# Optimization experiments

Hardware: AMD Instinct MI355X
Metric: run time of the kernel (lower is better)

Reference implementation:

```python
import jax, jax.numpy as jnp
import numpy as np

N = 100000; E = 200000; H = 64; P2 = 250000; P3 = 500000; G = 2048; NC = 10
NF = 18; EF = 18; Y = 0.25; EPS_BN = 1e-5


def setup_inputs() -> dict:
    key = jax.random.key(0)
    ks = jax.random.split(key, 20)
    def rn(i, shape, s=0.05):
        return jax.random.normal(ks[i], shape, jnp.float32) * s
    inp = {}
    inp["x"] = jax.random.normal(ks[0], (N, NF), jnp.float32)
    inp["edge_attr"] = jax.random.normal(ks[1], (E, EF), jnp.float32)
    inp["paths2"] = jax.random.randint(ks[2], (P2, 2), 0, N, jnp.int32)
    inp["ei2"] = jax.random.randint(ks[3], (P2, 1), 0, E, jnp.int32)
    inp["paths3"] = jax.random.randint(ks[4], (P3, 3), 0, N, jnp.int32)
    inp["ei3"] = jax.random.randint(ks[5], (P3, 2), 0, E, jnp.int32)
    inp["batch"] = jnp.sort(jax.random.randint(ks[6], (N,), 0, G, jnp.int32))
    inp["w_feat"] = rn(7, (NF, H)); inp["b_feat"] = jnp.zeros((H,), jnp.float32)
    inp["w_bond"] = rn(8, (EF, H)); inp["b_bond"] = jnp.zeros((H,), jnp.float32)
    inp["w_ih"] = rn(9, (4 * H, 2 * H)); inp["w_hh"] = rn(10, (4 * H, H))
    inp["b_ih"] = jnp.zeros((4 * H,), jnp.float32); inp["b_hh"] = jnp.zeros((4 * H,), jnp.float32)
    inp["bn_g"] = jnp.ones((2, H), jnp.float32); inp["bn_b"] = jnp.zeros((2, H), jnp.float32)
    inp["mlp_w1"] = rn(11, (2, H, H)); inp["mlp_b1"] = jnp.zeros((2, H), jnp.float32)
    inp["bn1_g"] = jnp.ones((2, H), jnp.float32); inp["bn1_b"] = jnp.zeros((2, H), jnp.float32)
    inp["mlp_w2"] = rn(12, (2, H, H)); inp["mlp_b2"] = jnp.zeros((2, H), jnp.float32)
    inp["bn2_g"] = jnp.ones((2, H), jnp.float32); inp["bn2_b"] = jnp.zeros((2, H), jnp.float32)
    inp["w_att"] = rn(13, (H,)); inp["b_att"] = jnp.zeros((1,), jnp.float32)
    inp["w_l1"] = rn(14, (H, H)); inp["b_l1"] = jnp.zeros((H,), jnp.float32)
    inp["w_l2"] = rn(15, (H, NC)); inp["b_l2"] = jnp.zeros((NC,), jnp.float32)
    return inp


def _batch_norm(x, g, b):
    # training-mode BN: biased batch statistics, eps=1e-5 (torch BatchNorm1d)
    m = x.mean(axis=0)
    v = x.var(axis=0)
    return (x - m) * jax.lax.rsqrt(v + EPS_BN) * g + b


def _lstm_final(x_seq, w_ih, w_hh, b_ih, b_hh):
    # x_seq: [P, L, 2H]; torch LSTM gate order i,f,g,o; return final hidden [P, H]
    P = x_seq.shape[0]
    Hd = w_hh.shape[1]
    def step(carry, xt):
        h, c = carry
        gates = xt @ w_ih.T + b_ih + h @ w_hh.T + b_hh
        i, f, g, o = jnp.split(gates, 4, axis=-1)
        c = jax.nn.sigmoid(f) * c + jax.nn.sigmoid(i) * jnp.tanh(g)
        h = jax.nn.sigmoid(o) * jnp.tanh(c)
        return (h, c), None
    h0 = jnp.zeros((P, Hd), x_seq.dtype)
    (h, _), _ = jax.lax.scan(step, (h0, h0), jnp.swapaxes(x_seq, 0, 1))
    return h


def _conv(i, x_in, ea_enc, paths, ei, w_ih, w_hh, b_ih, b_hh, bn_g, bn_b,
          mlp_w1, mlp_b1, bn1_g, bn1_b, mlp_w2, mlp_b2, bn2_g, bn2_b):
    P = paths.shape[0]
    ea = ea_enc[ei]                                        # [P, L-1, H]
    ea = jnp.concatenate([jnp.zeros((P, 1, H), ea.dtype), ea], axis=1)  # [P, L, H]
    x_cat = jnp.concatenate([x_in[paths], ea], axis=-1)    # [P, L, 2H]
    h = _lstm_final(x_cat, w_ih, w_hh, b_ih, b_hh)         # [P, H]
    h = jax.ops.segment_sum(h, paths[:, -1], num_segments=N)  # scatter_add to nodes
    h = _batch_norm(h, bn_g[i], bn_b[i])                   # residuals=False
    h = jax.nn.relu(_batch_norm(h @ mlp_w1[i] + mlp_b1[i], bn1_g[i], bn1_b[i]))
    h = jax.nn.relu(_batch_norm(h @ mlp_w2[i] + mlp_b2[i], bn2_g[i], bn2_b[i]))
    return h


def _attention(query, keys, w_att, b_att):
    scores = []
    for k in keys:
        s = jnp.sum(query * k, axis=0)                     # [H], sum over nodes
        s = (s - s.min()) / (s.max() - s.min() + 1e-6)
        scores.append(s @ w_att + b_att[0])                # scalar
    w = jax.nn.softmax(jnp.stack(scores))                  # [K]
    rep = sum(k * w[j] for j, k in enumerate(keys))
    return rep + query


def _forward(x, edge_attr, w_feat, b_feat, w_bond, b_bond, w_ih, w_hh, b_ih, b_hh,
             bn_g, bn_b, mlp_w1, mlp_b1, bn1_g, bn1_b, mlp_w2, mlp_b2, bn2_g, bn2_b,
             w_att, b_att, w_l1, b_l1, w_l2, b_l2, paths2, ei2, paths3, ei3, batch):
    W0 = x @ w_feat + b_feat                               # [N, H]
    ea_enc = edge_attr @ w_bond + b_bond                   # [E, H]
    common = (w_ih, w_hh, b_ih, b_hh, bn_g, bn_b, mlp_w1, mlp_b1, bn1_g, bn1_b,
              mlp_w2, mlp_b2, bn2_g, bn2_b)
    W1 = _conv(0, W0, ea_enc, paths2, ei2, *common)
    Win = (1.0 - Y) * W0 - Y * W1
    W2 = _conv(1, Win, ea_enc, paths3, ei3, *common)
    out = _attention(W0, [W1, W2], w_att, b_att)           # [N, H]
    out = jax.ops.segment_sum(out, batch, num_segments=G)  # global_add_pool -> [G, H]
    out = jax.nn.relu(out @ w_l1 + b_l1)
    return out @ w_l2 + b_l2                               # [G, NC]


def reference(x, edge_attr, paths2, ei2, paths3, ei3, batch, w_feat, b_feat,
              w_bond, b_bond, w_ih, w_hh, b_ih, b_hh, bn_g, bn_b, mlp_w1, mlp_b1,
              bn1_g, bn1_b, mlp_w2, mlp_b2, bn2_g, bn2_b, w_att, b_att,
              w_l1, b_l1, w_l2, b_l2):
    return _forward(x, edge_attr, w_feat, b_feat, w_bond, b_bond, w_ih, w_hh, b_ih, b_hh,
                    bn_g, bn_b, mlp_w1, mlp_b1, bn1_g, bn1_b, mlp_w2, mlp_b2, bn2_g, bn2_b,
                    w_att, b_att, w_l1, b_l1, w_l2, b_l2, paths2, ei2, paths3, ei3, batch)
```

## Files before the change

kernel.cpp:

```cpp
#include <hip/hip_runtime.h>
#include <math.h>

#define NNODES 100000
#define NEDGES 200000
#define HD 64
#define NP2 250000
#define NP3 500000
#define NG 2048
#define NCLS 10
#define NFEAT 18
#define EFEAT 18

typedef short short8v __attribute__((ext_vector_type(8)));
typedef float f32x4 __attribute__((ext_vector_type(4)));

__device__ __forceinline__ unsigned short bf16r(float a) {
    unsigned u = __builtin_bit_cast(unsigned, a);
    return (unsigned short)((u + 0x7FFFu + ((u >> 16) & 1u)) >> 16);
}

#define LOG2E 1.4426950408889634f

__global__ void prep_all(const float* __restrict__ w_ih, const float* __restrict__ w_hh,
                         const float* __restrict__ b_ih, const float* __restrict__ b_hh,
                         unsigned short* __restrict__ Bp, float* __restrict__ bsum,
                         float* __restrict__ zsmall, float* __restrict__ pooled) {
    int b = blockIdx.x;
    int t = threadIdx.x;
    if (b < 192) {
        int gid = b * 256 + t;
        int kc = gid >> 13;
        int rem = gid & 8191;
        int nt = rem >> 9;
        int rem2 = rem & 511;
        int l = rem2 >> 3, j = rem2 & 7;
        int c = l & 15, q = l >> 4;
        int jh = nt >> 2, qg = nt & 3;
        int k = kc * 32 + q * 8 + j;
        int n = qg * 64 + 16 * jh + c;
        float f = (k < 128) ? w_ih[n * 128 + k] : w_hh[n * 64 + (k - 128)];
        float s = (qg == 2) ? 2.f * LOG2E : LOG2E;
        Bp[gid] = bf16r(f * s);
    } else if (b == 192) {
        float s = ((t >> 6) == 2) ? 2.f * LOG2E : LOG2E;
        bsum[t] = (b_ih[t] + b_hh[t]) * s;
        for (int i = t; i < 960; i += 256) zsmall[i] = 0.f;
    } else {
        pooled[(b - 193) * 256 + t] = 0.f;
    }
}

__global__ void encode_all(const float* __restrict__ X, const float* __restrict__ Wf,
                           const float* __restrict__ bf,
                           const float* __restrict__ Ea, const float* __restrict__ Wb,
                           const float* __restrict__ bb,
                           float* __restrict__ W0, unsigned short* __restrict__ W0b,
                           unsigned short* __restrict__ eab) {
    long gid = (long)blockIdx.x * 256 + threadIdx.x;
    if (gid >= (long)(NNODES + NEDGES) * 64) return;
    long r = gid >> 6;
    int col = (int)(gid & 63);
    if (r < NNODES) {
        float acc = bf[col];
        const float* xr = X + r * NFEAT;
        for (int k = 0; k < NFEAT; ++k) acc += xr[k] * Wf[k * 64 + col];
        W0[gid] = acc;
        W0b[gid] = bf16r(acc);
    } else {
        long r2 = r - NNODES;
        float acc = bb[col];
        const float* xr = Ea + r2 * EFEAT;
        for (int k = 0; k < EFEAT; ++k) acc += xr[k] * Wb[k * 64 + col];
        eab[r2 * 64 + col] = bf16r(acc);
    }
}

template <int L>
__global__ __launch_bounds__(256, 3)
void conv_mfma(const unsigned short* __restrict__ xb, const unsigned short* __restrict__ eab,
               const int* __restrict__ paths, const int* __restrict__ ei,
               const unsigned short* __restrict__ Bp, const float* __restrict__ bsum,
               float* __restrict__ hsum, int P) {
    __shared__ unsigned short Al[2][64 * 200];

    const int t = threadIdx.x;
    const int w = t >> 6, lane = t & 63;
    const int c = lane & 15, q = lane >> 4;
    const int pl = t >> 2, gq = t & 3;
    const long pg = (long)blockIdx.x * 64 + pl;
    const int pc = (pg < P) ? (int)pg : P - 1;

    const short8v* __restrict__ Bv = (const short8v*)Bp;
    const int bbase = w * 256 + lane;

    short8v Bk0[4];
#pragma unroll
    for (int g2 = 0; g2 < 4; ++g2) Bk0[g2] = Bv[g2 * 64 + bbase];
    f32x4 bfr[4];
#pragma unroll
    for (int g2 = 0; g2 < 4; ++g2) {
        float b = bsum[g2 * 64 + 16 * w + c];
        f32x4 v; v[0] = b; v[1] = b; v[2] = b; v[3] = b;
        bfr[g2] = v;
    }

    float creg[16];
#pragma unroll
    for (int i = 0; i < 16; ++i) creg[i] = 0.f;

    f32x4 acc[4][4];
    short8v s0[4], s1[4];
    uint4 nu0, nu1, ev0, ev1;

    {
        int node = paths[pc * L + 0];
        const uint4* s4 = (const uint4*)(xb + (size_t)node * HD);
        *(uint4*)&Al[0][pl * 200 + gq * 16] = s4[2 * gq];
        *(uint4*)&Al[0][pl * 200 + gq * 16 + 8] = s4[2 * gq + 1];
    }
    __syncthreads();

#define LOADB(BUF, KC)                                                         \
        { _Pragma("unroll")                                                    \
          for (int g2 = 0; g2 < 4; ++g2)                                       \
              BUF[g2] = Bv[(KC) * 1024 + g2 * 64 + bbase]; }

#define CHUNKB(BUF, KC)                                                        \
        { _Pragma("unroll")                                                    \
          for (int mt = 0; mt < 4; ++mt) {                                     \
              short8v af = *(const short8v*)&Ac[(mt * 16 + c) * 200 + (KC) * 32 + q * 8]; \
              _Pragma("unroll")                                                \
              for (int g2 = 0; g2 < 4; ++g2)                                   \
                  acc[mt][g2] = __builtin_amdgcn_mfma_f32_16x16x32_bf16(       \
                      af, BUF[g2], bfr[g2], 0, 0, 0);                          \
          } }

#define CHUNKS(BUF, KC)                                                        \
        { _Pragma("unroll")                                                    \
          for (int mt = 0; mt < 4; ++mt) {                                     \
              short8v af = *(const short8v*)&Ac[(mt * 16 + c) * 200 + (KC) * 32 + q * 8]; \
              _Pragma("unroll")                                                \
              for (int g2 = 0; g2 < 4; ++g2)                                   \
                  acc[mt][g2] = __builtin_amdgcn_mfma_f32_16x16x32_bf16(       \
                      af, BUF[g2], acc[mt][g2], 0, 0, 0);                      \
          } }

    int cur = 0;
    for (int step = 0; step < L; ++step) {
        const unsigned short* Ac = Al[cur];
        unsigned short* An = Al[cur ^ 1];

        if (step == 0) {
            LOADB(s0, 1)
            CHUNKB(Bk0, 0)
            CHUNKS(s0, 1)
        } else {
            LOADB(s0, 1) LOADB(s1, 2)
            CHUNKB(Bk0, 0)
            CHUNKS(s0, 1) LOADB(s0, 3)
            CHUNKS(s1, 2) LOADB(s1, 4)
            CHUNKS(s0, 3) LOADB(s0, 5)
            CHUNKS(s1, 4)
            CHUNKS(s0, 5)
        }

        if (step + 1 < L) {
            int node = paths[pc * L + step + 1];
            const uint4* s4 = (const uint4*)(xb + (size_t)node * HD);
            nu0 = s4[2 * gq]; nu1 = s4[2 * gq + 1];
            int e = ei[pc * (L - 1) + step];
            const uint4* e4 = (const uint4*)(eab + (size_t)e * HD);
            ev0 = e4[2 * gq]; ev1 = e4[2 * gq + 1];
        }

#pragma unroll
        for (int mt = 0; mt < 4; ++mt) {
#pragma unroll
            for (int r = 0; r < 4; ++r) {
                float gi = acc[mt][0][r], gf = acc[mt][1][r];
                float gg = acc[mt][2][r], go = acc[mt][3][r];
                float ea = __builtin_amdgcn_exp2f(-gf);
                float eb = __builtin_amdgcn_exp2f(-gi);
                float ed = __builtin_amdgcn_exp2f(-gg);
                float eo = __builtin_amdgcn_exp2f(-go);
                float pa = 1.f + ea, pb = 1.f + eb, pd = 1.f + ed;
                float cn = (creg[mt * 4 + r] * pb * pd + (1.f - ed) * pa) *
                           __builtin_amdgcn_rcpf(pa * pb * pd);
                creg[mt * 4 + r] = cn;
                float et = __builtin_amdgcn_exp2f(-2.8853900817779268f * cn);
                float hn = (1.f - et) *
                           __builtin_amdgcn_rcpf((1.f + eo) * (1.f + et));
                if (step < L - 1) {
                    An[(mt * 16 + q * 4 + r) * 200 + 128 + 16 * w + c] = bf16r(hn);
                } else {
                    long pr = (long)blockIdx.x * 64 + mt * 16 + q * 4 + r;
                    if (pr < P) {
                        int node = paths[pr * L + (L - 1)];
                        atomicAdd(hsum + (size_t)node * HD + 16 * w + c, hn);
                    }
                }
            }
        }

        if (step + 1 < L) {
            *(uint4*)&An[pl * 200 + gq * 16] = nu0;
            *(uint4*)&An[pl * 200 + gq * 16 + 8] = nu1;
            *(uint4*)&An[pl * 200 + 64 + gq * 16] = ev0;
            *(uint4*)&An[pl * 200 + 64 + gq * 16 + 8] = ev1;
            __syncthreads();
        }
        cur ^= 1;
    }
#undef LOADB
#undef CHUNKB
#undef CHUNKS
}

__global__ void col_stats(const float* __restrict__ X, int nrows, float* __restrict__ out) {
    int col = threadIdx.x & 63, rg = threadIdx.x >> 6;
    float s = 0.f, q = 0.f;
    long stride = (long)gridDim.x * 4;
    for (long r = (long)blockIdx.x * 4 + rg; r < nrows; r += stride) {
        float v = X[r * 64 + col];
        s += v;
        q += v * v;
    }
    __shared__ float red[2][256];
    red[0][threadIdx.x] = s;
    red[1][threadIdx.x] = q;
    __syncthreads();
    if (threadIdx.x < 64) {
        int c = threadIdx.x;
        float ss = red[0][c] + red[0][c + 64] + red[0][c + 128] + red[0][c + 192];
        float qq = red[1][c] + red[1][c + 64] + red[1][c + 128] + red[1][c + 192];
        atomicAdd(out + c, ss);
        atomicAdd(out + 64 + c, qq);
    }
}

__device__ __forceinline__ void bn_affine(const float* stats, const float* g,
                                          const float* b, int col, int nrows,
                                          float& a, float& c) {
    float inv = 1.0f / (float)nrows;
    float mean = stats[col] * inv;
    float var = stats[64 + col] * inv - mean * mean;
    a = g[col] * rsqrtf(var + 1e-5f);
    c = b[col] - mean * a;
}

template <bool INRELU, bool STATS>
__global__ __launch_bounds__(256)
void gemm64(const float* __restrict__ X, const float* __restrict__ stats_in,
            const float* __restrict__ bn_gm, const float* __restrict__ bn_bt,
            const float* __restrict__ W, const float* __restrict__ bias,
            float* __restrict__ Y, float* stats, int nrows) {
    __shared__ float Xs[64 * 64];
    __shared__ float red[2][256];
    const int t = threadIdx.x;
    const int col = t & 63, rg = t >> 6;
    const long r0 = (long)blockIdx.x * 64;

    float a = 1.f, c = 0.f;
    if (stats_in) bn_affine(stats_in, bn_gm, bn_bt, col, nrows, a, c);

    for (int i = 0; i < 16; ++i) {
        int rl = rg * 16 + i;
        long r = r0 + rl;
        float v = (r < nrows) ? X[r * 64 + col] : 0.f;
        v = v * a + c;
        if (INRELU) v = fmaxf(v, 0.f);
        Xs[rl * 64 + col] = v;
    }
    __syncthreads();

    float wreg[64];
#pragma unroll
    for (int k = 0; k < 64; ++k) wreg[k] = W[k * 64 + col];
    float bs = bias[col];
    float ssum = 0.f, ssq = 0.f;

    for (int i = 0; i < 16; ++i) {
        int rl = rg * 16 + i;
        long r = r0 + rl;
        const float4* xs4 = (const float4*)(Xs + rl * 64);
        float acc = bs;
#pragma unroll
        for (int k4 = 0; k4 < 16; ++k4) {
            float4 xv = xs4[k4];
            acc += xv.x * wreg[4 * k4] + xv.y * wreg[4 * k4 + 1] +
                   xv.z * wreg[4 * k4 + 2] + xv.w * wreg[4 * k4 + 3];
        }
        if (r < nrows) {
            Y[r * 64 + col] = acc;
            ssum += acc;
            ssq += acc * acc;
        }
    }
    if (STATS) {
        red[0][t] = ssum;
        red[1][t] = ssq;
        __syncthreads();
        if (t < 64) {
            float s = red[0][t] + red[0][t + 64] + red[0][t + 128] + red[0][t + 192];
            float qq = red[1][t] + red[1][t + 64] + red[1][t + 128] + red[1][t + 192];
            atomicAdd(stats + t, s);
            atomicAdd(stats + 64 + t, qq);
        }
    }
}

__global__ void bn_apply1(float* __restrict__ W1, const float* __restrict__ stats,
                          const float* __restrict__ g, const float* __restrict__ b,
                          const float* __restrict__ W0, unsigned short* __restrict__ Winb,
                          long n) {
    long gid = (long)blockIdx.x * 256 + threadIdx.x;
    if (gid >= n * 64) return;
    int col = (int)(gid & 63);
    float a, c;
    bn_affine(stats, g, b, col, (int)n, a, c);
    float v = fmaxf(W1[gid] * a + c, 0.f);
    W1[gid] = v;
    Winb[gid] = bf16r(0.75f * W0[gid] - 0.25f * v);
}

__global__ void bn_apply_att(float* __restrict__ W2, const float* __restrict__ stats,
                             const float* __restrict__ g, const float* __restrict__ b,
                             const float* __restrict__ W0, const float* __restrict__ W1,
                             float* __restrict__ atts, int n) {
    int col = threadIdx.x & 63, rg = threadIdx.x >> 6;
    float a, c;
    bn_affine(stats, g, b, col, n, a, c);
    float s1 = 0.f, s2 = 0.f;
    long stride = (long)gridDim.x * 4;
    for (long r = (long)blockIdx.x * 4 + rg; r < n; r += stride) {
        long gid = r * 64 + col;
        float v = fmaxf(W2[gid] * a + c, 0.f);
        W2[gid] = v;
        float q0 = W0[gid];
        s1 += q0 * W1[gid];
        s2 += q0 * v;
    }
    __shared__ float red[2][256];
    red[0][threadIdx.x] = s1;
    red[1][threadIdx.x] = s2;
    __syncthreads();
    if (threadIdx.x < 64) {
        int cc = threadIdx.x;
        float a1 = red[0][cc] + red[0][cc + 64] + red[0][cc + 128] + red[0][cc + 192];
        float a2 = red[1][cc] + red[1][cc + 64] + red[1][cc + 128] + red[1][cc + 192];
        atomicAdd(atts + cc, a1);
        atomicAdd(atts + 64 + cc, a2);
    }
}

#define PROWS 128
__global__ void pool_rep(const float* __restrict__ W0, const float* __restrict__ W1,
                         const float* __restrict__ W2, const float* __restrict__ atts,
                         const float* __restrict__ w_att, const float* __restrict__ b_att,
                         const int* __restrict__ batch, float* __restrict__ pooled, int n) {
    __shared__ float wsh[2];
    if (threadIdx.x < 64) {
        int h = threadIdx.x;
        float z[2];
        for (int k = 0; k < 2; ++k) {
            float s = atts[64 * k + h];
            float mn = s, mx = s;
            for (int off = 32; off > 0; off >>= 1) {
                mn = fminf(mn, __shfl_down(mn, off));
                mx = fmaxf(mx, __shfl_down(mx, off));
            }
            mn = __shfl(mn, 0);
            mx = __shfl(mx, 0);
            float sn = (s - mn) / (mx - mn + 1e-6f);
            float d = sn * w_att[h];
            for (int off = 32; off > 0; off >>= 1) d += __shfl_down(d, off);
            z[k] = __shfl(d, 0) + b_att[0];
        }
        if (h == 0) {
            float m = fmaxf(z[0], z[1]);
            float e0 = expf(z[0] - m), e1 = expf(z[1] - m);
            float inv = 1.0f / (e0 + e1);
            wsh[0] = e0 * inv;
            wsh[1] = e1 * inv;
        }
    }
    __syncthreads();
    int col = threadIdx.x & 63, rg = threadIdx.x >> 6;
    long r0 = (long)blockIdx.x * PROWS;
    float w1 = wsh[0], w2 = wsh[1];
    float acc = 0.f;
    int curg = -1;
    for (int i = rg; i < PROWS; i += 4) {
        long r = r0 + i;
        if (r >= n) break;
        int g = batch[r];
        long gid = r * 64 + col;
        float rep = W0[gid] + w1 * W1[gid] + w2 * W2[gid];
        if (g != curg) {
            if (curg >= 0) atomicAdd(pooled + (size_t)curg * 64 + col, acc);
            curg = g;
            acc = 0.f;
        }
        acc += rep;
    }
    if (curg >= 0) atomicAdd(pooled + (size_t)curg * 64 + col, acc);
}

__global__ __launch_bounds__(256)
void head_kernel(const float* __restrict__ pooled, const float* __restrict__ w_l1,
                 const float* __restrict__ b_l1, const float* __restrict__ w_l2,
                 const float* __restrict__ b_l2, float* __restrict__ out) {
    __shared__ float Xs[64 * 64];
    __shared__ float Ys[64 * 65];
    const int t = threadIdx.x;
    const int col = t & 63, rg = t >> 6;
    const int r0 = blockIdx.x * 64;

    for (int i = 0; i < 16; ++i) {
        int rl = rg * 16 + i;
        Xs[rl * 64 + col] = fmaxf(pooled[(size_t)(r0 + rl) * 64 + col], 0.f);
    }
    __syncthreads();

    float wreg[64];
#pragma unroll
    for (int k = 0; k < 64; ++k) wreg[k] = w_l1[k * 64 + col];
    float bs = b_l1[col];

    for (int i = 0; i < 16; ++i) {
        int rl = rg * 16 + i;
        const float4* xs4 = (const float4*)(Xs + rl * 64);
        float acc = bs;
#pragma unroll
        for (int k4 = 0; k4 < 16; ++k4) {
            float4 xv = xs4[k4];
            acc += xv.x * wreg[4 * k4] + xv.y * wreg[4 * k4 + 1] +
                   xv.z * wreg[4 * k4 + 2] + xv.w * wreg[4 * k4 + 3];
        }
        Ys[rl * 65 + col] = fmaxf(acc, 0.f);
    }
    __syncthreads();

    for (int idx = t; idx < 64 * NCLS; idx += 256) {
        int row = idx / NCLS, j = idx - row * NCLS;
        float acc = b_l2[j];
#pragma unroll
        for (int k = 0; k < 64; ++k) acc += Ys[row * 65 + k] * w_l2[k * NCLS + j];
        out[(size_t)(r0 + row) * NCLS + j] = acc;
    }
}

extern "C" void kernel_launch(void* const* d_in, const int* in_sizes, int n_in,
                              void* d_out, int out_size, void* d_ws, size_t ws_size,
                              hipStream_t stream) {
    const float* x         = (const float*)d_in[0];
    const float* edge_attr = (const float*)d_in[1];
    const int*   paths2    = (const int*)d_in[2];
    const int*   ei2       = (const int*)d_in[3];
    const int*   paths3    = (const int*)d_in[4];
    const int*   ei3       = (const int*)d_in[5];
    const int*   batch     = (const int*)d_in[6];
    const float* w_feat    = (const float*)d_in[7];
    const float* b_feat    = (const float*)d_in[8];
    const float* w_bond    = (const float*)d_in[9];
    const float* b_bond    = (const float*)d_in[10];
    const float* w_ih      = (const float*)d_in[11];
    const float* w_hh      = (const float*)d_in[12];
    const float* b_ih      = (const float*)d_in[13];
    const float* b_hh      = (const float*)d_in[14];
    const float* bn_g      = (const float*)d_in[15];
    const float* bn_b      = (const float*)d_in[16];
    const float* mlp_w1    = (const float*)d_in[17];
    const float* mlp_b1    = (const float*)d_in[18];
    const float* bn1_g     = (const float*)d_in[19];
    const float* bn1_b     = (const float*)d_in[20];
    const float* mlp_w2    = (const float*)d_in[21];
    const float* mlp_b2    = (const float*)d_in[22];
    const float* bn2_g     = (const float*)d_in[23];
    const float* bn2_b     = (const float*)d_in[24];
    const float* w_att     = (const float*)d_in[25];
    const float* b_att     = (const float*)d_in[26];
    const float* w_l1      = (const float*)d_in[27];
    const float* b_l1      = (const float*)d_in[28];
    const float* w_l2      = (const float*)d_in[29];
    const float* b_l2      = (const float*)d_in[30];

    const size_t N64 = (size_t)NNODES * 64;
    float* ws = (float*)d_ws;
    float* W0     = ws;
    float* W1     = W0 + N64;
    float* W2     = W1 + N64;
    float* Wtmp   = W2 + N64;
    float* hsum1  = Wtmp + N64;
    float* hsum2  = hsum1 + N64;
    unsigned short* W0b  = (unsigned short*)(hsum2 + N64);
    unsigned short* Winb = W0b + N64;
    unsigned short* eab  = Winb + N64;
    unsigned short* Bp   = eab + (size_t)NEDGES * 64;
    float* bsum   = (float*)(Bp + 6 * 16 * 64 * 8);
    float* st     = bsum + 256;
    float* atts   = st + 6 * 128;
    float* watt   = atts + 128;
    float* pooled = watt + 64;

    hipMemsetAsync(hsum1, 0, 2 * N64 * sizeof(float), stream);

    prep_all<<<193 + 512, 256, 0, stream>>>(w_ih, w_hh, b_ih, b_hh, Bp, bsum, st, pooled);
    encode_all<<<(int)(((size_t)(NNODES + NEDGES) * 64 + 255) / 256), 256, 0, stream>>>(
        x, w_feat, b_feat, edge_attr, w_bond, b_bond, W0, W0b, eab);

    conv_mfma<2><<<(NP2 + 63) / 64, 256, 0, stream>>>(W0b, eab, paths2, ei2, Bp, bsum, hsum1, NP2);

    col_stats<<<1024, 256, 0, stream>>>(hsum1, NNODES, st + 0);
    gemm64<false, true><<<(NNODES + 63) / 64, 256, 0, stream>>>(hsum1, st + 0, bn_g + 0, bn_b + 0, mlp_w1, mlp_b1, Wtmp, st + 128, NNODES);
    gemm64<true, true><<<(NNODES + 63) / 64, 256, 0, stream>>>(Wtmp, st + 128, bn1_g + 0, bn1_b + 0, mlp_w2, mlp_b2, W1, st + 256, NNODES);
    bn_apply1<<<(NNODES * 64 + 255) / 256, 256, 0, stream>>>(W1, st + 256, bn2_g + 0, bn2_b + 0, W0, Winb, NNODES);

    conv_mfma<3><<<(NP3 + 63) / 64, 256, 0, stream>>>(Winb, eab, paths3, ei3, Bp, bsum, hsum2, NP3);

    col_stats<<<1024, 256, 0, stream>>>(hsum2, NNODES, st + 384);
    gemm64<false, true><<<(NNODES + 63) / 64, 256, 0, stream>>>(hsum2, st + 384, bn_g + 64, bn_b + 64, mlp_w1 + 4096, mlp_b1 + 64, Wtmp, st + 512, NNODES);
    gemm64<true, true><<<(NNODES + 63) / 64, 256, 0, stream>>>(Wtmp, st + 512, bn1_g + 64, bn1_b + 64, mlp_w2 + 4096, mlp_b2 + 64, W2, st + 640, NNODES);
    bn_apply_att<<<1024, 256, 0, stream>>>(W2, st + 640, bn2_g + 64, bn2_b + 64, W0, W1, atts, NNODES);

    pool_rep<<<(NNODES + PROWS - 1) / PROWS, 256, 0, stream>>>(W0, W1, W2, atts, w_att, b_att, batch, pooled, NNODES);
    head_kernel<<<NG / 64, 256, 0, stream>>>(pooled, w_l1, b_l1, w_l2, b_l2, (float*)d_out);
}
```

Before: 775.7 us.

## Prefetch path indices and issue next-step gathers before MFMA chunks in LSTM conv

All path node and edge indices are loaded into registers up front, and the gather of the next step's node/edge features is issued before the MFMA chunk sequence instead of after it, so global memory latency overlaps with matrix compute. The weight loads are deepened to three staging buffers, and the gate nonlinearity is rewritten on float2 vectors to encourage packed FP32 math. This raises register pressure under the 3-blocks-per-SM launch bound, which could cause spills or lower occupancy.

```diff
diff --git a/kernel.cpp b/kernel.cpp
--- a/kernel.cpp
+++ b/kernel.cpp
@@ -13,6 +13,7 @@
 
 typedef short short8v __attribute__((ext_vector_type(8)));
 typedef float f32x4 __attribute__((ext_vector_type(4)));
+typedef float f32x2 __attribute__((ext_vector_type(2)));
 
 __device__ __forceinline__ unsigned short bf16r(float a) {
     unsigned u = __builtin_bit_cast(unsigned, a);
@@ -93,6 +94,13 @@
     const short8v* __restrict__ Bv = (const short8v*)Bp;
     const int bbase = w * 256 + lane;
 
+    int nidx[L];
+#pragma unroll
+    for (int s = 0; s < L; ++s) nidx[s] = paths[pc * L + s];
+    int eidx[L - 1];
+#pragma unroll
+    for (int s = 0; s + 1 < L; ++s) eidx[s] = ei[pc * (L - 1) + s];
+
     short8v Bk0[4];
 #pragma unroll
     for (int g2 = 0; g2 < 4; ++g2) Bk0[g2] = Bv[g2 * 64 + bbase];
@@ -109,12 +117,11 @@
     for (int i = 0; i < 16; ++i) creg[i] = 0.f;
 
     f32x4 acc[4][4];
-    short8v s0[4], s1[4];
+    short8v s0[4], s1[4], s2[4];
     uint4 nu0, nu1, ev0, ev1;
 
     {
-        int node = paths[pc * L + 0];
-        const uint4* s4 = (const uint4*)(xb + (size_t)node * HD);
+        const uint4* s4 = (const uint4*)(xb + (size_t)nidx[0] * HD);
         *(uint4*)&Al[0][pl * 200 + gq * 16] = s4[2 * gq];
         *(uint4*)&Al[0][pl * 200 + gq * 16 + 8] = s4[2 * gq + 1];
     }
@@ -145,6 +152,14 @@
                       af, BUF[g2], acc[mt][g2], 0, 0, 0);                      \
           } }
 
+#define GATHER(S)                                                              \
+        {                                                                      \
+            const uint4* s4 = (const uint4*)(xb + (size_t)nidx[(S)] * HD);     \
+            nu0 = s4[2 * gq]; nu1 = s4[2 * gq + 1];                            \
+            const uint4* e4 = (const uint4*)(eab + (size_t)eidx[(S) - 1] * HD);\
+            ev0 = e4[2 * gq]; ev1 = e4[2 * gq + 1];                            \
+        }
+
     int cur = 0;
     for (int step = 0; step < L; ++step) {
         const unsigned short* Ac = Al[cur];
@@ -152,51 +167,63 @@
 
         if (step == 0) {
             LOADB(s0, 1)
+            GATHER(1)
             CHUNKB(Bk0, 0)
             CHUNKS(s0, 1)
         } else {
-            LOADB(s0, 1) LOADB(s1, 2)
+            LOADB(s0, 1) LOADB(s1, 2) LOADB(s2, 3)
+            if (step + 1 < L) GATHER(step + 1)
             CHUNKB(Bk0, 0)
-            CHUNKS(s0, 1) LOADB(s0, 3)
-            CHUNKS(s1, 2) LOADB(s1, 4)
-            CHUNKS(s0, 3) LOADB(s0, 5)
-            CHUNKS(s1, 4)
-            CHUNKS(s0, 5)
-        }
-
-        if (step + 1 < L) {
-            int node = paths[pc * L + step + 1];
-            const uint4* s4 = (const uint4*)(xb + (size_t)node * HD);
-            nu0 = s4[2 * gq]; nu1 = s4[2 * gq + 1];
-            int e = ei[pc * (L - 1) + step];
-            const uint4* e4 = (const uint4*)(eab + (size_t)e * HD);
-            ev0 = e4[2 * gq]; ev1 = e4[2 * gq + 1];
+            CHUNKS(s0, 1) LOADB(s0, 4)
+            CHUNKS(s1, 2) LOADB(s1, 5)
+            CHUNKS(s2, 3)
+            CHUNKS(s0, 4)
+            CHUNKS(s1, 5)
         }
 
 #pragma unroll
         for (int mt = 0; mt < 4; ++mt) {
 #pragma unroll
-            for (int r = 0; r < 4; ++r) {
-                float gi = acc[mt][0][r], gf = acc[mt][1][r];
-                float gg = acc[mt][2][r], go = acc[mt][3][r];
-                float ea = __builtin_amdgcn_exp2f(-gf);
-                float eb = __builtin_amdgcn_exp2f(-gi);
-                float ed = __builtin_amdgcn_exp2f(-gg);
-                float eo = __builtin_amdgcn_exp2f(-go);
-                float pa = 1.f + ea, pb = 1.f + eb, pd = 1.f + ed;
-                float cn = (creg[mt * 4 + r] * pb * pd + (1.f - ed) * pa) *
-                           __builtin_amdgcn_rcpf(pa * pb * pd);
-                creg[mt * 4 + r] = cn;
-                float et = __builtin_amdgcn_exp2f(-2.8853900817779268f * cn);
-                float hn = (1.f - et) *
-                           __builtin_amdgcn_rcpf((1.f + eo) * (1.f + et));
+            for (int rp = 0; rp < 2; ++rp) {
+                const int r0i = rp * 2;
+                f32x2 gi = {acc[mt][0][r0i], acc[mt][0][r0i + 1]};
+                f32x2 gf = {acc[mt][1][r0i], acc[mt][1][r0i + 1]};
+                f32x2 gg = {acc[mt][2][r0i], acc[mt][2][r0i + 1]};
+                f32x2 go = {acc[mt][3][r0i], acc[mt][3][r0i + 1]};
+                f32x2 ea, eb, ed, eo;
+                ea.x = __builtin_amdgcn_exp2f(-gf.x); ea.y = __builtin_amdgcn_exp2f(-gf.y);
+                eb.x = __builtin_amdgcn_exp2f(-gi.x); eb.y = __builtin_amdgcn_exp2f(-gi.y);
+                ed.x = __builtin_amdgcn_exp2f(-gg.x); ed.y = __builtin_amdgcn_exp2f(-gg.y);
+                eo.x = __builtin_amdgcn_exp2f(-go.x); eo.y = __builtin_amdgcn_exp2f(-go.y);
+                f32x2 pa = ea + 1.f, pb = eb + 1.f, pd = ed + 1.f;
+                f32x2 cr = {creg[mt * 4 + r0i], creg[mt * 4 + r0i + 1]};
+                f32x2 pbpd = pb * pd;
+                f32x2 num = cr * pbpd + (1.f - ed) * pa;
+                f32x2 den = pa * pbpd;
+                f32x2 cn;
+                cn.x = num.x * __builtin_amdgcn_rcpf(den.x);
+                cn.y = num.y * __builtin_amdgcn_rcpf(den.y);
+                creg[mt * 4 + r0i] = cn.x;
+                creg[mt * 4 + r0i + 1] = cn.y;
+                f32x2 arg = cn * -2.8853900817779268f;
+                f32x2 et;
+                et.x = __builtin_amdgcn_exp2f(arg.x); et.y = __builtin_amdgcn_exp2f(arg.y);
+                f32x2 den2 = (eo + 1.f) * (et + 1.f);
+                f32x2 hn;
+                hn.x = (1.f - et.x) * __builtin_amdgcn_rcpf(den2.x);
+                hn.y = (1.f - et.y) * __builtin_amdgcn_rcpf(den2.y);
                 if (step < L - 1) {
-                    An[(mt * 16 + q * 4 + r) * 200 + 128 + 16 * w + c] = bf16r(hn);
+                    An[(mt * 16 + q * 4 + r0i) * 200 + 128 + 16 * w + c] = bf16r(hn.x);
+                    An[(mt * 16 + q * 4 + r0i + 1) * 200 + 128 + 16 * w + c] = bf16r(hn.y);
                 } else {
-                    long pr = (long)blockIdx.x * 64 + mt * 16 + q * 4 + r;
-                    if (pr < P) {
-                        int node = paths[pr * L + (L - 1)];
-                        atomicAdd(hsum + (size_t)node * HD + 16 * w + c, hn);
+                    long pr0 = (long)blockIdx.x * 64 + mt * 16 + q * 4 + r0i;
+                    if (pr0 < P) {
+                        int node = paths[pr0 * L + (L - 1)];
+                        atomicAdd(hsum + (size_t)node * HD + 16 * w + c, hn.x);
+                    }
+                    if (pr0 + 1 < P) {
+                        int node = paths[(pr0 + 1) * L + (L - 1)];
+                        atomicAdd(hsum + (size_t)node * HD + 16 * w + c, hn.y);
                     }
                 }
             }
@@ -214,6 +241,7 @@
 #undef LOADB
 #undef CHUNKB
 #undef CHUNKS
+#undef GATHER
 }
 
 __global__ void col_stats(const float* __restrict__ X, int nrows, float* __restrict__ out) {
```

New measurement: 795.6 us. 1.03x slower.

## Fuse prep, encode and memset into one launch; reschedule conv gather loads

Applied to the files above, without the earlier changes.

Merges the weight-packing, encoder and hsum zeroing (previously a hipMemsetAsync) into a single kernel launch, removing two launches and their gaps. In the LSTM conv kernel, the next-step node and edge gathers are issued earlier (during step 0 and mid-MFMA chain) to hide global-load latency, with a three-buffer B fragment rotation. The last-node index for the atomic scatter is cached in shared memory instead of re-read from global. The extra B buffer raises register pressure, which could hurt occupancy under launch_bounds(256,3).

```diff
diff --git a/kernel.cpp b/kernel.cpp
--- a/kernel.cpp
+++ b/kernel.cpp
@@ -21,14 +21,41 @@
 
 #define LOG2E 1.4426950408889634f
 
-__global__ void prep_all(const float* __restrict__ w_ih, const float* __restrict__ w_hh,
-                         const float* __restrict__ b_ih, const float* __restrict__ b_hh,
-                         unsigned short* __restrict__ Bp, float* __restrict__ bsum,
-                         float* __restrict__ zsmall, float* __restrict__ pooled) {
+#define NB_ENC (((NNODES + NEDGES) * 64 + 255) / 256)
+
+__global__ void prep_encode(const float* __restrict__ X, const float* __restrict__ Wf,
+                            const float* __restrict__ bf,
+                            const float* __restrict__ Ea, const float* __restrict__ Wb,
+                            const float* __restrict__ bb,
+                            float* __restrict__ W0, unsigned short* __restrict__ W0b,
+                            unsigned short* __restrict__ eab,
+                            const float* __restrict__ w_ih, const float* __restrict__ w_hh,
+                            const float* __restrict__ b_ih, const float* __restrict__ b_hh,
+                            unsigned short* __restrict__ Bp, float* __restrict__ bsum,
+                            float* __restrict__ zsmall, float* __restrict__ hzero,
+                            float* __restrict__ pooled) {
     int b = blockIdx.x;
     int t = threadIdx.x;
-    if (b < 192) {
-        int gid = b * 256 + t;
+    if (b < NB_ENC) {
+        long gid = (long)b * 256 + t;
+        if (gid >= (long)(NNODES + NEDGES) * 64) return;
+        long r = gid >> 6;
+        int col = (int)(gid & 63);
+        if (r < NNODES) {
+            float acc = bf[col];
+            const float* xr = X + r * NFEAT;
+            for (int k = 0; k < NFEAT; ++k) acc += xr[k] * Wf[k * 64 + col];
+            W0[gid] = acc;
+            W0b[gid] = bf16r(acc);
+        } else {
+            long r2 = r - NNODES;
+            float acc = bb[col];
+            const float* xr = Ea + r2 * EFEAT;
+            for (int k = 0; k < EFEAT; ++k) acc += xr[k] * Wb[k * 64 + col];
+            eab[r2 * 64 + col] = bf16r(acc);
+        }
+    } else if (b < NB_ENC + 192) {
+        int gid = (b - NB_ENC) * 256 + t;
         int kc = gid >> 13;
         int rem = gid & 8191;
         int nt = rem >> 9;
@@ -41,37 +68,18 @@
         float f = (k < 128) ? w_ih[n * 128 + k] : w_hh[n * 64 + (k - 128)];
         float s = (qg == 2) ? 2.f * LOG2E : LOG2E;
         Bp[gid] = bf16r(f * s);
-    } else if (b == 192) {
+    } else if (b == NB_ENC + 192) {
         float s = ((t >> 6) == 2) ? 2.f * LOG2E : LOG2E;
         bsum[t] = (b_ih[t] + b_hh[t]) * s;
         for (int i = t; i < 960; i += 256) zsmall[i] = 0.f;
+    } else if (b < NB_ENC + 193 + 3200) {
+        long base = ((long)(b - NB_ENC - 193) * 256 + t) * 16;
+        f32x4 z = {0.f, 0.f, 0.f, 0.f};
+        f32x4* p = (f32x4*)(hzero + base);
+        long lim = 2L * NNODES * 64;
+        if (base + 16 <= lim) { p[0] = z; p[1] = z; p[2] = z; p[3] = z; }
     } else {
-        pooled[(b - 193) * 256 + t] = 0.f;
-    }
-}
-
-__global__ void encode_all(const float* __restrict__ X, const float* __restrict__ Wf,
-                           const float* __restrict__ bf,
-                           const float* __restrict__ Ea, const float* __restrict__ Wb,
-                           const float* __restrict__ bb,
-                           float* __restrict__ W0, unsigned short* __restrict__ W0b,
-                           unsigned short* __restrict__ eab) {
-    long gid = (long)blockIdx.x * 256 + threadIdx.x;
-    if (gid >= (long)(NNODES + NEDGES) * 64) return;
-    long r = gid >> 6;
-    int col = (int)(gid & 63);
-    if (r < NNODES) {
-        float acc = bf[col];
-        const float* xr = X + r * NFEAT;
-        for (int k = 0; k < NFEAT; ++k) acc += xr[k] * Wf[k * 64 + col];
-        W0[gid] = acc;
-        W0b[gid] = bf16r(acc);
-    } else {
-        long r2 = r - NNODES;
-        float acc = bb[col];
-        const float* xr = Ea + r2 * EFEAT;
-        for (int k = 0; k < EFEAT; ++k) acc += xr[k] * Wb[k * 64 + col];
-        eab[r2 * 64 + col] = bf16r(acc);
+        pooled[(b - NB_ENC - 193 - 3200) * 256 + t] = 0.f;
     }
 }
 
@@ -82,6 +90,7 @@
                const unsigned short* __restrict__ Bp, const float* __restrict__ bsum,
                float* __restrict__ hsum, int P) {
     __shared__ unsigned short Al[2][64 * 200];
+    __shared__ int lastnode_s[64];
 
     const int t = threadIdx.x;
     const int w = t >> 6, lane = t & 63;
@@ -109,7 +118,7 @@
     for (int i = 0; i < 16; ++i) creg[i] = 0.f;
 
     f32x4 acc[4][4];
-    short8v s0[4], s1[4];
+    short8v bs0[4], bs1[4], bs2[4];
     uint4 nu0, nu1, ev0, ev1;
 
     {
@@ -117,6 +126,7 @@
         const uint4* s4 = (const uint4*)(xb + (size_t)node * HD);
         *(uint4*)&Al[0][pl * 200 + gq * 16] = s4[2 * gq];
         *(uint4*)&Al[0][pl * 200 + gq * 16 + 8] = s4[2 * gq + 1];
+        if (gq == 0) lastnode_s[pl] = paths[pc * L + (L - 1)];
     }
     __syncthreads();
 
@@ -151,26 +161,33 @@
         unsigned short* An = Al[cur ^ 1];
 
         if (step == 0) {
-            LOADB(s0, 1)
+            LOADB(bs0, 1)
+            {
+                int node = paths[pc * L + 1];
+                const uint4* s4 = (const uint4*)(xb + (size_t)node * HD);
+                nu0 = s4[2 * gq]; nu1 = s4[2 * gq + 1];
+                int e = ei[pc * (L - 1) + 0];
+                const uint4* e4 = (const uint4*)(eab + (size_t)e * HD);
+                ev0 = e4[2 * gq]; ev1 = e4[2 * gq + 1];
+            }
             CHUNKB(Bk0, 0)
-            CHUNKS(s0, 1)
+            CHUNKS(bs0, 1)
         } else {
-            LOADB(s0, 1) LOADB(s1, 2)
+            LOADB(bs0, 1) LOADB(bs1, 2) LOADB(bs2, 3)
             CHUNKB(Bk0, 0)
-            CHUNKS(s0, 1) LOADB(s0, 3)
-            CHUNKS(s1, 2) LOADB(s1, 4)
-            CHUNKS(s0, 3) LOADB(s0, 5)
-            CHUNKS(s1, 4)
-            CHUNKS(s0, 5)
-        }
-
-        if (step + 1 < L) {
-            int node = paths[pc * L + step + 1];
-            const uint4* s4 = (const uint4*)(xb + (size_t)node * HD);
-            nu0 = s4[2 * gq]; nu1 = s4[2 * gq + 1];
-            int e = ei[pc * (L - 1) + step];
-            const uint4* e4 = (const uint4*)(eab + (size_t)e * HD);
-            ev0 = e4[2 * gq]; ev1 = e4[2 * gq + 1];
+            CHUNKS(bs0, 1) LOADB(bs0, 4)
+            CHUNKS(bs1, 2) LOADB(bs1, 5)
+            CHUNKS(bs2, 3)
+            if (step + 1 < L) {
+                int node = paths[pc * L + step + 1];
+                const uint4* s4 = (const uint4*)(xb + (size_t)node * HD);
+                nu0 = s4[2 * gq]; nu1 = s4[2 * gq + 1];
+                int e = ei[pc * (L - 1) + step];
+                const uint4* e4 = (const uint4*)(eab + (size_t)e * HD);
+                ev0 = e4[2 * gq]; ev1 = e4[2 * gq + 1];
+            }
+            CHUNKS(bs0, 4)
+            CHUNKS(bs1, 5)
         }
 
 #pragma unroll
@@ -195,7 +212,7 @@
                 } else {
                     long pr = (long)blockIdx.x * 64 + mt * 16 + q * 4 + r;
                     if (pr < P) {
-                        int node = paths[pr * L + (L - 1)];
+                        int node = lastnode_s[mt * 16 + q * 4 + r];
                         atomicAdd(hsum + (size_t)node * HD + 16 * w + c, hn);
                     }
                 }
@@ -503,11 +520,9 @@
     float* watt   = atts + 128;
     float* pooled = watt + 64;
 
-    hipMemsetAsync(hsum1, 0, 2 * N64 * sizeof(float), stream);
-
-    prep_all<<<193 + 512, 256, 0, stream>>>(w_ih, w_hh, b_ih, b_hh, Bp, bsum, st, pooled);
-    encode_all<<<(int)(((size_t)(NNODES + NEDGES) * 64 + 255) / 256), 256, 0, stream>>>(
-        x, w_feat, b_feat, edge_attr, w_bond, b_bond, W0, W0b, eab);
+    prep_encode<<<NB_ENC + 193 + 3200 + 512, 256, 0, stream>>>(
+        x, w_feat, b_feat, edge_attr, w_bond, b_bond, W0, W0b, eab,
+        w_ih, w_hh, b_ih, b_hh, Bp, bsum, st, hsum1, pooled);
 
     conv_mfma<2><<<(NP2 + 63) / 64, 256, 0, stream>>>(W0b, eab, paths2, ei2, Bp, bsum, hsum1, NP2);
 
```

After: 767.8 us. No clear change (-1.0%).
